# Kernel optimization log

Measured on AMD Instinct MI355X. Metric: run time of the kernel, lower is better.

Reference implementation:

```python
import jax, jax.numpy as jnp
import numpy as np

B, S, K, N = 4, 2048, 4096, 4096
BLK = 32  # Q4_0 block size along the K (input) dimension


def setup_inputs() -> dict:
    key = jax.random.key(0)
    k1, k2, k3, k4 = jax.random.split(key, 4)
    x = jax.random.normal(k1, (B, S, K), dtype=jnp.float32)
    # 4-bit codes stored unpacked as int32 in [0, 16)
    qweight = jax.random.randint(k2, (N, K), 0, 16, dtype=jnp.int32)
    # one positive fp scale per 32-wide block (typical Q4_0 magnitudes)
    scales = jax.random.uniform(k3, (N, K // BLK), dtype=jnp.float32) * 0.1
    bias = jax.random.normal(k4, (N,), dtype=jnp.float32)
    return {"x": x, "qweight": qweight, "scales": scales, "bias": bias}


def dequantize_q4_0(qweight, scales):
    # w[n, k] = scale[n, k//32] * (q[n, k] - 8)
    n, k = qweight.shape
    q = qweight.reshape(n, k // BLK, BLK).astype(scales.dtype)
    w = (q - 8.0) * scales[:, :, None]
    return w.reshape(n, k)


def reference(x, qweight, scales, bias):
    # dequantize once (cached path), then F.linear(x, w, bias)
    w = dequantize_q4_0(qweight, scales)          # [N, K]
    out = jnp.einsum("bsk,nk->bsn", x, w)          # [B, S, N]
    return out + bias
```

## Files before the change

### kernel.cpp

```cpp
#include <hip/hip_runtime.h>
#include <stdint.h>

#define M_DIM 8192
#define N_DIM 4096
#define K_DIM 4096
#define NKB   (K_DIM / 32)
#define BK    64
#define KSTEPS (K_DIM / BK)

typedef __bf16 bf16x8 __attribute__((ext_vector_type(8)));
typedef float  f32x4  __attribute__((ext_vector_type(4)));

__device__ __forceinline__ uint32_t pack2_bf16(float lo, float hi) {
    union { float f; uint32_t u; } a, b;
    a.f = lo; b.f = hi;
    return __builtin_amdgcn_perm(b.u + 0x8000u, a.u + 0x8000u, 0x07060302u);
}


__global__ void cvt_x_kernel(const float* __restrict__ x,
                             uint32_t* __restrict__ xb, int n8) {
    int i = blockIdx.x * blockDim.x + threadIdx.x;
    if (i >= n8) return;
    const float4* p = (const float4*)x;
    float4 v0 = p[2 * i], v1 = p[2 * i + 1];
    uint4 o;
    o.x = pack2_bf16(v0.x, v0.y);
    o.y = pack2_bf16(v0.z, v0.w);
    o.z = pack2_bf16(v1.x, v1.y);
    o.w = pack2_bf16(v1.z, v1.w);
    ((uint4*)xb)[i] = o;
}

__global__ void dequant_kernel(const int* __restrict__ q,
                               const float* __restrict__ s,
                               uint32_t* __restrict__ wb, int n8) {
    int i = blockIdx.x * blockDim.x + threadIdx.x;
    if (i >= n8) return;
    int base = i << 3;
    int n = base >> 12;
    int k = base & (K_DIM - 1);
    float sc = s[n * NKB + (k >> 5)];
    float m8 = -8.0f * sc;
    const int4* qp = (const int4*)q;
    int4 q0 = qp[2 * i], q1 = qp[2 * i + 1];
    uint4 o;
    o.x = pack2_bf16(fmaf((float)q0.x, sc, m8), fmaf((float)q0.y, sc, m8));
    o.y = pack2_bf16(fmaf((float)q0.z, sc, m8), fmaf((float)q0.w, sc, m8));
    o.z = pack2_bf16(fmaf((float)q1.x, sc, m8), fmaf((float)q1.y, sc, m8));
    o.w = pack2_bf16(fmaf((float)q1.z, sc, m8), fmaf((float)q1.w, sc, m8));
    ((uint4*)wb)[i] = o;
}

__global__ __launch_bounds__(256)
void gemm_bf16_kernel(const __bf16* __restrict__ A,
                      const __bf16* __restrict__ Bw,
                      const float* __restrict__ bias,
                      float* __restrict__ C) {
    __shared__ __align__(16) __bf16 lA[128 * BK];
    __shared__ __align__(16) __bf16 lB[128 * BK];

    const int t    = threadIdx.x;
    const int wave = t >> 6;
    const int lane = t & 63;
    const int bm = blockIdx.y, bn = blockIdx.x;
    const int wm = wave >> 1, wn = wave & 1;

    const int trow = t >> 3;
    const int cg   = (t & 7) ^ (trow & 7);
    const __bf16* gA = A  + (size_t)(bm * 128 + trow) * K_DIM + cg * 8;
    const __bf16* gB = Bw + (size_t)(bn * 128 + trow) * K_DIM + cg * 8;

#define ISSUE_LOADS()                                                         \
    do {                                                                      \
        _Pragma("unroll")                                                     \
        for (int kk = 0; kk < 4; ++kk) {                                      \
            __builtin_amdgcn_global_load_lds(                                 \
                (const __attribute__((address_space(1))) uint32_t*)           \
                    (gA + (size_t)(32 * kk) * K_DIM),                         \
                (__attribute__((address_space(3))) uint32_t*)                 \
                    (lA + (t + 256 * kk) * 8), 16, 0, 0);                     \
            __builtin_amdgcn_global_load_lds(                                 \
                (const __attribute__((address_space(1))) uint32_t*)           \
                    (gB + (size_t)(32 * kk) * K_DIM),                         \
                (__attribute__((address_space(3))) uint32_t*)                 \
                    (lB + (t + 256 * kk) * 8), 16, 0, 0);                     \
        }                                                                     \
    } while (0)

    const int r = lane & 15, quad = lane >> 4;
    const int s0 = quad ^ (r & 7);
    const __bf16* fA = lA + (wm * 64 + r) * BK;
    const __bf16* fB = lB + (wn * 64 + r) * BK;

    f32x4 acc[4][4] = {};

    ISSUE_LOADS();

    for (int kt = 0; kt < KSTEPS; ++kt) {
        __syncthreads();
        bf16x8 af[2][4], bfr[2][4];
#pragma unroll
        for (int i = 0; i < 4; ++i) {
            af[0][i]  = *(const bf16x8*)(fA + i * 16 * BK + s0 * 8);
            af[1][i]  = *(const bf16x8*)(fA + i * 16 * BK + (s0 ^ 4) * 8);
            bfr[0][i] = *(const bf16x8*)(fB + i * 16 * BK + s0 * 8);
            bfr[1][i] = *(const bf16x8*)(fB + i * 16 * BK + (s0 ^ 4) * 8);
        }
        __syncthreads();

        if (kt + 1 < KSTEPS) {
            gA += BK; gB += BK;
            ISSUE_LOADS();
        }

#pragma unroll
        for (int h = 0; h < 2; ++h)
#pragma unroll
            for (int i = 0; i < 4; ++i)
#pragma unroll
                for (int j = 0; j < 4; ++j)
                    acc[i][j] = __builtin_amdgcn_mfma_f32_16x16x32_bf16(
                        af[h][i], bfr[h][j], acc[i][j], 0, 0, 0);
    }
#undef ISSUE_LOADS

    const int m0 = bm * 128 + wm * 64;
    const int n0 = bn * 128 + wn * 64;
#pragma unroll
    for (int j = 0; j < 4; ++j) {
        int col = n0 + j * 16 + r;
        float bv = bias[col];
#pragma unroll
        for (int i = 0; i < 4; ++i) {
            int rbase = m0 + i * 16 + quad * 4;
#pragma unroll
            for (int e = 0; e < 4; ++e)
                C[(size_t)(rbase + e) * N_DIM + col] = acc[i][j][e] + bv;
        }
    }
}

__global__ __launch_bounds__(256)
void fused_gemm_kernel(const float* __restrict__ X,
                       const int* __restrict__ Q,
                       const float* __restrict__ S,
                       const float* __restrict__ bias,
                       float* __restrict__ C) {
    __shared__ __align__(16) __bf16 lA[128 * 32];
    __shared__ __align__(16) __bf16 lB[128 * 32];

    const int t    = threadIdx.x;
    const int wave = t >> 6;
    const int lane = t & 63;
    const int bm = blockIdx.y, bn = blockIdx.x;
    const int wm = wave >> 1, wn = wave & 1;

    const int srow = t >> 1;
    const int sc0  = (t & 1) << 4;
    const float* gX = X + (size_t)(bm * 128 + srow) * K_DIM + sc0;
    const int*   gQ = Q + (size_t)(bn * 128 + srow) * K_DIM + sc0;
    const float* gS = S + (size_t)(bn * 128 + srow) * NKB;
    __bf16* sA = lA + srow * 32 + sc0;
    __bf16* sB = lB + srow * 32 + sc0;

    const int r = lane & 15, quad = lane >> 4;
    const __bf16* fA = lA + (wm * 64 + r) * 32 + quad * 8;
    const __bf16* fB = lB + (wn * 64 + r) * 32 + quad * 8;

    f32x4 acc[4][4] = {};

    float4 x0 = ((const float4*)gX)[0];
    float4 x1 = ((const float4*)gX)[1];
    float4 x2 = ((const float4*)gX)[2];
    float4 x3 = ((const float4*)gX)[3];
    int4 q0 = ((const int4*)gQ)[0];
    int4 q1 = ((const int4*)gQ)[1];
    int4 q2 = ((const int4*)gQ)[2];
    int4 q3 = ((const int4*)gQ)[3];
    float sc = gS[0];

    for (int kt = 0; kt < NKB; ++kt) {
        uint4 pa0, pa1, pb0, pb1;
        pa0.x = pack2_bf16(x0.x, x0.y); pa0.y = pack2_bf16(x0.z, x0.w);
        pa0.z = pack2_bf16(x1.x, x1.y); pa0.w = pack2_bf16(x1.z, x1.w);
        pa1.x = pack2_bf16(x2.x, x2.y); pa1.y = pack2_bf16(x2.z, x2.w);
        pa1.z = pack2_bf16(x3.x, x3.y); pa1.w = pack2_bf16(x3.z, x3.w);
        float m8 = -8.0f * sc;
        pb0.x = pack2_bf16(fmaf((float)q0.x, sc, m8), fmaf((float)q0.y, sc, m8));
        pb0.y = pack2_bf16(fmaf((float)q0.z, sc, m8), fmaf((float)q0.w, sc, m8));
        pb0.z = pack2_bf16(fmaf((float)q1.x, sc, m8), fmaf((float)q1.y, sc, m8));
        pb0.w = pack2_bf16(fmaf((float)q1.z, sc, m8), fmaf((float)q1.w, sc, m8));
        pb1.x = pack2_bf16(fmaf((float)q2.x, sc, m8), fmaf((float)q2.y, sc, m8));
        pb1.y = pack2_bf16(fmaf((float)q2.z, sc, m8), fmaf((float)q2.w, sc, m8));
        pb1.z = pack2_bf16(fmaf((float)q3.x, sc, m8), fmaf((float)q3.y, sc, m8));
        pb1.w = pack2_bf16(fmaf((float)q3.z, sc, m8), fmaf((float)q3.w, sc, m8));

        __syncthreads();
        *(uint4*)sA = pa0; *(uint4*)(sA + 8) = pa1;
        *(uint4*)sB = pb0; *(uint4*)(sB + 8) = pb1;
        __syncthreads();

        if (kt + 1 < NKB) {
            gX += 32; gQ += 32;
            x0 = ((const float4*)gX)[0];
            x1 = ((const float4*)gX)[1];
            x2 = ((const float4*)gX)[2];
            x3 = ((const float4*)gX)[3];
            q0 = ((const int4*)gQ)[0];
            q1 = ((const int4*)gQ)[1];
            q2 = ((const int4*)gQ)[2];
            q3 = ((const int4*)gQ)[3];
            sc = gS[kt + 1];
        }

        bf16x8 af[4], bfr[4];
#pragma unroll
        for (int i = 0; i < 4; ++i)
            af[i] = *(const bf16x8*)(fA + i * 16 * 32);
#pragma unroll
        for (int j = 0; j < 4; ++j)
            bfr[j] = *(const bf16x8*)(fB + j * 16 * 32);
#pragma unroll
        for (int i = 0; i < 4; ++i)
#pragma unroll
            for (int j = 0; j < 4; ++j)
                acc[i][j] = __builtin_amdgcn_mfma_f32_16x16x32_bf16(
                    af[i], bfr[j], acc[i][j], 0, 0, 0);
    }

    const int m0 = bm * 128 + wm * 64;
    const int n0 = bn * 128 + wn * 64;
#pragma unroll
    for (int j = 0; j < 4; ++j) {
        int col = n0 + j * 16 + r;
        float bv = bias[col];
#pragma unroll
        for (int i = 0; i < 4; ++i) {
            int rbase = m0 + i * 16 + quad * 4;
#pragma unroll
            for (int e = 0; e < 4; ++e)
                C[(size_t)(rbase + e) * N_DIM + col] = acc[i][j][e] + bv;
        }
    }
}

extern "C" void kernel_launch(void* const* d_in, const int* in_sizes, int n_in,
                              void* d_out, int out_size, void* d_ws, size_t ws_size,
                              hipStream_t stream) {
    const float* x    = (const float*)d_in[0];
    const int*   qw   = (const int*)d_in[1];
    const float* sc   = (const float*)d_in[2];
    const float* bias = (const float*)d_in[3];
    float* out = (float*)d_out;

    dim3 grid(N_DIM / 128, M_DIM / 128);

    const size_t need = ((size_t)M_DIM * K_DIM + (size_t)N_DIM * K_DIM) * 2;
    if (ws_size >= need && d_ws != nullptr) {
        uint32_t* xb = (uint32_t*)d_ws;
        uint32_t* wb = xb + (size_t)M_DIM * K_DIM / 2;
        int n8x = M_DIM * K_DIM / 8;
        cvt_x_kernel<<<n8x / 256, 256, 0, stream>>>(x, xb, n8x);
        int n8w = N_DIM * K_DIM / 8;
        dequant_kernel<<<n8w / 256, 256, 0, stream>>>(qw, sc, wb, n8w);
        gemm_bf16_kernel<<<grid, 256, 0, stream>>>(
            (const __bf16*)xb, (const __bf16*)wb, bias, out);
    } else {
        fused_gemm_kernel<<<grid, 256, 0, stream>>>(x, qw, sc, bias, out);
    }
}
```

Baseline: 548.2 us.

## Replace 128x128 GEMM with 256x256 tile, 8-wave pipelined schedule and XCD-aware remap

The bf16 GEMM is rewritten to use 256x256 output tiles with 512 threads (8 waves). LDS is split into double-buffered A and B halves, and global-to-LDS loads are interleaved with MFMA phases using explicit barriers, vmcnt waits and setprio. Workgroup ids are remapped so that consecutive tiles spread across the 8 XCDs. The aim is to raise arithmetic intensity and overlap memory traffic with compute, at the cost of heavy register pressure (128 accumulator floats per lane) and 128KB of LDS per workgroup, which may limit occupancy.

```diff
diff --git a/kernel.cpp b/kernel.cpp
--- a/kernel.cpp
+++ b/kernel.cpp
@@ -6,7 +6,9 @@
 #define K_DIM 4096
 #define NKB   (K_DIM / 32)
 #define BK    64
-#define KSTEPS (K_DIM / BK)
+#define KT    (K_DIM / BK)
+#define ITERS (KT / 2)
+#define GRID_WGS ((M_DIM / 256) * (N_DIM / 256))
 
 typedef __bf16 bf16x8 __attribute__((ext_vector_type(8)));
 typedef float  f32x4  __attribute__((ext_vector_type(4)));
@@ -52,88 +54,158 @@
     ((uint4*)wb)[i] = o;
 }
 
-__global__ __launch_bounds__(256)
-void gemm_bf16_kernel(const __bf16* __restrict__ A,
-                      const __bf16* __restrict__ Bw,
-                      const float* __restrict__ bias,
-                      float* __restrict__ C) {
-    __shared__ __align__(16) __bf16 lA[128 * BK];
-    __shared__ __align__(16) __bf16 lB[128 * BK];
+__global__ __launch_bounds__(512, 2)
+void gemm_bf16_256_kernel(const __bf16* __restrict__ A,
+                          const __bf16* __restrict__ Bw,
+                          const float* __restrict__ bias,
+                          float* __restrict__ C) {
+    __shared__ __align__(16) __bf16 lds[8][128 * 64];
 
     const int t    = threadIdx.x;
     const int wave = t >> 6;
     const int lane = t & 63;
-    const int bm = blockIdx.y, bn = blockIdx.x;
-    const int wm = wave >> 1, wn = wave & 1;
-
-    const int trow = t >> 3;
-    const int cg   = (t & 7) ^ (trow & 7);
-    const __bf16* gA = A  + (size_t)(bm * 128 + trow) * K_DIM + cg * 8;
-    const __bf16* gB = Bw + (size_t)(bn * 128 + trow) * K_DIM + cg * 8;
-
-#define ISSUE_LOADS()                                                         \
+    const int wm = wave >> 2;
+    const int wn = wave & 3;
+
+    const int flat = blockIdx.x;
+    const int wgid = (flat & 7) * (GRID_WGS / 8) + (flat >> 3);
+    const int bm = wgid >> 4;
+    const int bn = wgid & 15;
+
+    const __bf16* Ab = A  + (size_t)bm * 256 * K_DIM;
+    const __bf16* Bb = Bw + (size_t)bn * 256 * K_DIM;
+
+    const int rr0 = t >> 3;
+    const int cg  = (t & 7) ^ (rr0 & 7);
+    const size_t aoff = (size_t)rr0 * K_DIM + cg * 8;
+    const size_t boff = (size_t)((rr0 >> 5) * 64 + (rr0 & 31)) * K_DIM + cg * 8;
+
+#define STAGE(ktg, unit)                                                      \
     do {                                                                      \
-        _Pragma("unroll")                                                     \
-        for (int kk = 0; kk < 4; ++kk) {                                      \
-            __builtin_amdgcn_global_load_lds(                                 \
-                (const __attribute__((address_space(1))) uint32_t*)           \
-                    (gA + (size_t)(32 * kk) * K_DIM),                         \
-                (__attribute__((address_space(3))) uint32_t*)                 \
-                    (lA + (t + 256 * kk) * 8), 16, 0, 0);                     \
-            __builtin_amdgcn_global_load_lds(                                 \
-                (const __attribute__((address_space(1))) uint32_t*)           \
-                    (gB + (size_t)(32 * kk) * K_DIM),                         \
-                (__attribute__((address_space(3))) uint32_t*)                 \
-                    (lB + (t + 256 * kk) * 8), 16, 0, 0);                     \
+        const __bf16* _s;                                                     \
+        __bf16* _d;                                                           \
+        if ((unit) == 0 || (unit) == 3) {                                     \
+            const int _mh = ((unit) == 3) ? 1 : 0;                            \
+            _s = Ab + (size_t)_mh * 64 * K_DIM + (size_t)(ktg) * 64 + aoff;   \
+            _d = &lds[((ktg) & 1) * 4 + _mh][0] + t * 8;                      \
+        } else {                                                              \
+            const int _nh = ((unit) == 2) ? 1 : 0;                            \
+            _s = Bb + (size_t)_nh * 32 * K_DIM + (size_t)(ktg) * 64 + boff;   \
+            _d = &lds[((ktg) & 1) * 4 + 2 + _nh][0] + t * 8;                  \
         }                                                                     \
+        __builtin_amdgcn_global_load_lds(                                     \
+            (const __attribute__((address_space(1))) uint32_t*)_s,            \
+            (__attribute__((address_space(3))) uint32_t*)_d, 16, 0, 0);       \
+        __builtin_amdgcn_global_load_lds(                                     \
+            (const __attribute__((address_space(1))) uint32_t*)               \
+                (_s + (size_t)128 * K_DIM),                                   \
+            (__attribute__((address_space(3))) uint32_t*)(_d + 4096),         \
+            16, 0, 0);                                                        \
     } while (0)
 
     const int r = lane & 15, quad = lane >> 4;
     const int s0 = quad ^ (r & 7);
-    const __bf16* fA = lA + (wm * 64 + r) * BK;
-    const __bf16* fB = lB + (wn * 64 + r) * BK;
-
-    f32x4 acc[4][4] = {};
-
-    ISSUE_LOADS();
-
-    for (int kt = 0; kt < KSTEPS; ++kt) {
-        __syncthreads();
-        bf16x8 af[2][4], bfr[2][4];
-#pragma unroll
-        for (int i = 0; i < 4; ++i) {
-            af[0][i]  = *(const bf16x8*)(fA + i * 16 * BK + s0 * 8);
-            af[1][i]  = *(const bf16x8*)(fA + i * 16 * BK + (s0 ^ 4) * 8);
-            bfr[0][i] = *(const bf16x8*)(fB + i * 16 * BK + s0 * 8);
-            bfr[1][i] = *(const bf16x8*)(fB + i * 16 * BK + (s0 ^ 4) * 8);
-        }
-        __syncthreads();
-
-        if (kt + 1 < KSTEPS) {
-            gA += BK; gB += BK;
-            ISSUE_LOADS();
-        }
-
-#pragma unroll
-        for (int h = 0; h < 2; ++h)
-#pragma unroll
-            for (int i = 0; i < 4; ++i)
-#pragma unroll
-                for (int j = 0; j < 4; ++j)
-                    acc[i][j] = __builtin_amdgcn_mfma_f32_16x16x32_bf16(
-                        af[h][i], bfr[h][j], acc[i][j], 0, 0, 0);
-    }
-#undef ISSUE_LOADS
-
-    const int m0 = bm * 128 + wm * 64;
-    const int n0 = bn * 128 + wn * 64;
+    const int aRow = (wm * 64 + r) * 64;
+    const int bRow = (wn * 32 + r) * 64;
+
+    bf16x8 a[4][2], b0[2][2], b1[2][2];
+    f32x4 acc[8][4] = {};
+
+#define LOAD_A(buf, mh)                                                       \
+    do { const __bf16* _p = &lds[(buf) * 4 + (mh)][aRow];                     \
+        _Pragma("unroll") for (int i2 = 0; i2 < 4; ++i2) {                    \
+            a[i2][0] = *(const bf16x8*)(_p + i2 * 1024 + s0 * 8);             \
+            a[i2][1] = *(const bf16x8*)(_p + i2 * 1024 + (s0 ^ 4) * 8);       \
+        } } while (0)
+
+#define LOAD_B(dst, buf, nh)                                                  \
+    do { const __bf16* _p = &lds[(buf) * 4 + 2 + (nh)][bRow];                 \
+        _Pragma("unroll") for (int j2 = 0; j2 < 2; ++j2) {                    \
+            dst[j2][0] = *(const bf16x8*)(_p + j2 * 1024 + s0 * 8);           \
+            dst[j2][1] = *(const bf16x8*)(_p + j2 * 1024 + (s0 ^ 4) * 8);     \
+        } } while (0)
+
+#define MFMA16(IB, BSEL, JB)                                                  \
+    do { __builtin_amdgcn_s_setprio(1);                                       \
+        _Pragma("unroll") for (int i2 = 0; i2 < 4; ++i2)                      \
+        _Pragma("unroll") for (int j2 = 0; j2 < 2; ++j2)                      \
+        _Pragma("unroll") for (int h = 0; h < 2; ++h)                         \
+            acc[(IB) + i2][(JB) + j2] =                                       \
+                __builtin_amdgcn_mfma_f32_16x16x32_bf16(                      \
+                    a[i2][h], BSEL[j2][h], acc[(IB) + i2][(JB) + j2],         \
+                    0, 0, 0);                                                 \
+        __builtin_amdgcn_s_setprio(0); } while (0)
+
+#define BAR() do { asm volatile("" ::: "memory");                             \
+                   __builtin_amdgcn_s_barrier();                              \
+                   asm volatile("" ::: "memory"); } while (0)
+#define VMCNT(n) asm volatile("s_waitcnt vmcnt(" #n ")" ::: "memory")
+
+    STAGE(0, 0); STAGE(0, 1); STAGE(0, 2); STAGE(0, 3);
+    STAGE(1, 0); STAGE(1, 1); STAGE(1, 2);
+    VMCNT(6);
+    BAR();
+
+#define KBODY(it, LAST)                                                       \
+    do {                                                                      \
+        const int _k0 = 2 * (it);                                             \
+                             \
+        LOAD_A(0, 0); LOAD_B(b0, 0, 0);                                       \
+        STAGE(_k0 + 1, 3);                                                    \
+        BAR(); MFMA16(0, b0, 0); BAR();                                       \
+                         \
+        LOAD_B(b1, 0, 1);                                                     \
+        if (!(LAST)) STAGE(_k0 + 2, 0);                                       \
+        BAR(); MFMA16(0, b1, 2); BAR();                                       \
+                       \
+        LOAD_A(0, 1);                                                         \
+        if (!(LAST)) STAGE(_k0 + 2, 1);                                       \
+        BAR(); MFMA16(4, b1, 2); BAR();                                       \
+         \
+        if (!(LAST)) STAGE(_k0 + 2, 2);                                       \
+        BAR(); MFMA16(4, b0, 0);                                              \
+        if (LAST) { VMCNT(0); } else { VMCNT(6); }                            \
+        BAR();                                                                \
+                          \
+        LOAD_A(1, 0); LOAD_B(b0, 1, 0);                                       \
+        if (!(LAST)) STAGE(_k0 + 2, 3);                                       \
+        BAR(); MFMA16(0, b0, 0); BAR();                                       \
+                         \
+        LOAD_B(b1, 1, 1);                                                     \
+        if (!(LAST)) STAGE(_k0 + 3, 0);                                       \
+        BAR(); MFMA16(0, b1, 2); BAR();                                       \
+                               \
+        LOAD_A(1, 1);                                                         \
+        if (!(LAST)) STAGE(_k0 + 3, 1);                                       \
+        BAR(); MFMA16(4, b1, 2); BAR();                                       \
+         \
+        if (!(LAST)) STAGE(_k0 + 3, 2);                                       \
+        BAR(); MFMA16(4, b0, 0);                                              \
+        if (!(LAST)) { VMCNT(6); }                                            \
+        BAR();                                                                \
+    } while (0)
+
+#pragma unroll 1
+    for (int it = 0; it < ITERS - 1; ++it) KBODY(it, 0);
+    KBODY(ITERS - 1, 1);
+
+#undef KBODY
+#undef STAGE
+#undef LOAD_A
+#undef LOAD_B
+#undef MFMA16
+#undef BAR
+#undef VMCNT
+
+    const int m0 = bm * 256 + wm * 128;
+    const int n0 = bn * 256 + wn * 64;
 #pragma unroll
     for (int j = 0; j < 4; ++j) {
-        int col = n0 + j * 16 + r;
-        float bv = bias[col];
-#pragma unroll
-        for (int i = 0; i < 4; ++i) {
-            int rbase = m0 + i * 16 + quad * 4;
+        const int col = n0 + j * 16 + r;
+        const float bv = bias[col];
+#pragma unroll
+        for (int i = 0; i < 8; ++i) {
+            const int rbase = m0 + i * 16 + quad * 4;
 #pragma unroll
             for (int e = 0; e < 4; ++e)
                 C[(size_t)(rbase + e) * N_DIM + col] = acc[i][j][e] + bv;
@@ -254,8 +326,6 @@
     const float* bias = (const float*)d_in[3];
     float* out = (float*)d_out;
 
-    dim3 grid(N_DIM / 128, M_DIM / 128);
-
     const size_t need = ((size_t)M_DIM * K_DIM + (size_t)N_DIM * K_DIM) * 2;
     if (ws_size >= need && d_ws != nullptr) {
         uint32_t* xb = (uint32_t*)d_ws;
@@ -264,9 +334,10 @@
         cvt_x_kernel<<<n8x / 256, 256, 0, stream>>>(x, xb, n8x);
         int n8w = N_DIM * K_DIM / 8;
         dequant_kernel<<<n8w / 256, 256, 0, stream>>>(qw, sc, wb, n8w);
-        gemm_bf16_kernel<<<grid, 256, 0, stream>>>(
+        gemm_bf16_256_kernel<<<dim3(GRID_WGS), dim3(512), 0, stream>>>(
             (const __bf16*)xb, (const __bf16*)wb, bias, out);
     } else {
+        dim3 grid(N_DIM / 128, M_DIM / 128);
         fused_gemm_kernel<<<grid, 256, 0, stream>>>(x, qw, sc, bias, out);
     }
 }
```

After: 481.9 us. 1.14x faster.
